# Kernel optimization log

Measured on AMD Instinct MI355X. Metric: run time of the kernel, lower is better.

Reference implementation:

```python
import jax, jax.numpy as jnp
import numpy as np

NUM_EXPERTS = 8
TOP_K = 2
D_MODEL = 1024
EXPERT_CAP = 512  # dim_feedforward // num_experts = 4096 // 8
B, S = 4, 2048


def setup_inputs() -> dict:
    key = jax.random.key(0)
    ks = jax.random.split(key, 4)
    scale = 1.0 / np.sqrt(D_MODEL)
    x = jax.random.normal(ks[0], (B, S, D_MODEL), dtype=jnp.float32)
    gate_w = jax.random.normal(ks[1], (D_MODEL, NUM_EXPERTS), dtype=jnp.float32) * scale
    w1 = jax.random.normal(ks[2], (NUM_EXPERTS, D_MODEL, EXPERT_CAP), dtype=jnp.float32) * scale
    b1 = jnp.zeros((NUM_EXPERTS, EXPERT_CAP), dtype=jnp.float32)
    w2 = jax.random.normal(ks[3], (NUM_EXPERTS, EXPERT_CAP, D_MODEL), dtype=jnp.float32) * (1.0 / np.sqrt(EXPERT_CAP))
    b2 = jnp.zeros((NUM_EXPERTS, D_MODEL), dtype=jnp.float32)
    return {"x": x, "gate_w": gate_w, "w1": w1, "b1": b1, "w2": w2, "b2": b2}


def reference(x, gate_w, w1, b1, w2, b2):
    Bx, Sx, D = x.shape
    xt = x.reshape(-1, D)  # [N, D], N = B*S
    gates = jax.nn.softmax(xt @ gate_w, axis=-1)           # [N, E]
    topk_g, topk_i = jax.lax.top_k(gates, TOP_K)           # [N, K]
    # Faithful to source: every selected expert is scaled by the SUM of all top-k gates
    tok_w = topk_g.sum(axis=-1)                            # [N]
    sel = (topk_i[:, :, None] == jnp.arange(NUM_EXPERTS)[None, None, :]).any(axis=1)  # [N, E] bool
    # Dense per-expert MLP (E small), then mask-combine (scatter-add equivalent)
    h = jax.nn.gelu(jnp.einsum('nd,edh->enh', xt, w1) + b1[:, None, :], approximate=False)  # [E, N, H]
    y = jnp.einsum('enh,ehd->end', h, w2) + b2[:, None, :]  # [E, N, D]
    out = jnp.einsum('end,ne,n->nd', y, sel.astype(x.dtype), tok_w)  # [N, D]
    return out.reshape(Bx, Sx, D)
```

## Files before the change

kernel.cpp:

```cpp
#include <hip/hip_runtime.h>
#include <math.h>

#define N_TOK 8192
#define DM 1024
#define NE 8
#define HE 512
#define NPAIR 16384
#define MAXMB 264

#define BM 64
#define BN 128
#define BK 64
#define OSTR 136

#define GSTR 1028

typedef __bf16 bf16x8 __attribute__((ext_vector_type(8)));
typedef float f32x4 __attribute__((ext_vector_type(4)));

#define GLOBAL_AS __attribute__((address_space(1)))
#define LDS_AS    __attribute__((address_space(3)))

__device__ __forceinline__ void gl_lds16(const void* g, void* lds) {
    __builtin_amdgcn_global_load_lds((const GLOBAL_AS unsigned int*)g,
                                     (LDS_AS unsigned int*)lds, 16, 0, 0);
}

__device__ __forceinline__ unsigned short f2bf(float f) {
    unsigned int u = __float_as_uint(f);
    u += 0x7fffu + ((u >> 16) & 1u);
    return (unsigned short)(u >> 16);
}

__device__ __forceinline__ float gelu_exact(float v) {
    return 0.5f * v * (1.0f + erff(v * 0.70710678118654752440f));
}

__device__ __forceinline__ double shfl_xor_dbl(double v, int m) {
    long long l = __double_as_longlong(v);
    int lo = (int)(l & 0xffffffffll);
    int hi = (int)(l >> 32);
    lo = __shfl_xor(lo, m, 64);
    hi = __shfl_xor(hi, m, 64);
    return __longlong_as_double(((long long)hi << 32) | (unsigned long long)(unsigned int)lo);
}

__global__ __launch_bounds__(256) void prep_kernel(
        const float* __restrict__ x, const float* __restrict__ gw,
        const float* __restrict__ w1, const float* __restrict__ w2,
        unsigned short* __restrict__ xb,
        unsigned short* __restrict__ w1t, unsigned short* __restrict__ w2t,
        float* __restrict__ w_tok, int* __restrict__ e_sel) {
    __shared__ float smf[NE * GSTR];
    int bid = blockIdx.x;
    int tid = threadIdx.x;

    if (bid >= 2048) {
        int t = bid - 2048;
        int z = t >> 7;
        int idx = t & 127;
        int bx = idx & 7, by = idx >> 3;
        const float* src; unsigned short* dst; int R, C, c0, r0;
        if (z < 8) {
            src = w1 + (size_t)z * DM * HE; dst = w1t + (size_t)z * DM * HE;
            R = DM; C = HE; c0 = bx * 64; r0 = by * 64;
        } else {
            int e = z - 8;
            src = w2 + (size_t)e * HE * DM; dst = w2t + (size_t)e * HE * DM;
            R = HE; C = DM; c0 = by * 64; r0 = bx * 64;
        }
        float (*tile)[65] = (float(*)[65])smf;
        int tc = tid & 63, tg = tid >> 6;
        #pragma unroll
        for (int i = 0; i < 16; i++) {
            int r = tg * 16 + i;
            tile[r][tc] = src[(size_t)(r0 + r) * C + (c0 + tc)];
        }
        __syncthreads();
        #pragma unroll
        for (int i = 0; i < 16; i++) {
            int r = tg * 16 + i;
            dst[(size_t)(c0 + r) * R + (r0 + tc)] = f2bf(tile[tc][r]);
        }
        return;
    }

    float* gls = smf;
    for (int v = tid; v < 2048; v += 256) {
        float4 g4 = ((const float4*)gw)[v];
        int idx = v * 4;
        int d = idx >> 3;
        int e0 = idx & 7;
        gls[(e0    ) * GSTR + d] = g4.x;
        gls[(e0 + 1) * GSTR + d] = g4.y;
        gls[(e0 + 2) * GSTR + d] = g4.z;
        gls[(e0 + 3) * GSTR + d] = g4.w;
    }
    __syncthreads();

    int n = bid * 4 + (tid >> 6);
    int lane = tid & 63;
    const float4* xr = (const float4*)(x + (size_t)n * DM);
    ushort4* xw = (ushort4*)(xb + (size_t)n * DM);

    double s[NE];
    #pragma unroll
    for (int e = 0; e < NE; e++) s[e] = 0.0;

    #pragma unroll
    for (int i = 0; i < 4; i++) {
        float4 x4 = xr[i * 64 + lane];
        ushort4 o;
        o.x = f2bf(x4.x); o.y = f2bf(x4.y); o.z = f2bf(x4.z); o.w = f2bf(x4.w);
        xw[i * 64 + lane] = o;
        int d = (i * 64 + lane) * 4;
        #pragma unroll
        for (int e = 0; e < NE; e++) {
            float4 g4 = *(const float4*)(&gls[e * GSTR + d]);
            s[e] += (double)x4.x * (double)g4.x + (double)x4.y * (double)g4.y
                  + (double)x4.z * (double)g4.z + (double)x4.w * (double)g4.w;
        }
    }
    #pragma unroll
    for (int e = 0; e < NE; e++) {
        for (int off = 32; off > 0; off >>= 1)
            s[e] += shfl_xor_dbl(s[e], off);
    }
    if (lane == 0) {
        double m = s[0];
        for (int e = 1; e < NE; e++) if (s[e] > m) m = s[e];
        double sum = 0.0;
        for (int e = 0; e < NE; e++) sum += exp(s[e] - m);
        int i1 = 0; double v1 = s[0];
        for (int e = 1; e < NE; e++) if (s[e] > v1) { v1 = s[e]; i1 = e; }
        int i2 = -1; double v2 = -1e300;
        for (int e = 0; e < NE; e++) if (e != i1 && s[e] > v2) { v2 = s[e]; i2 = e; }
        w_tok[n] = (float)((exp(v1 - m) + exp(v2 - m)) / sum);
        e_sel[2 * n]     = i1;
        e_sel[2 * n + 1] = i2;
    }
}

__global__ __launch_bounds__(1024) void route_kernel(
        const int* __restrict__ e_sel, int* __restrict__ cnt, int* __restrict__ offs,
        int* __restrict__ pair_tok, int* __restrict__ slotmap,
        int* __restrict__ mb_e, int* __restrict__ mb_base, int* __restrict__ n_mb) {
    __shared__ int wbin[16][NE];
    __shared__ int wstart[16][NE];
    __shared__ int etot[NE], eoffs[NE], bofs[NE];
    int tid = threadIdx.x;
    int w = tid >> 6, l = tid & 63;
    if (l < NE) wbin[w][l] = 0;
    __syncthreads();

    int sel[16];
    #pragma unroll
    for (int k = 0; k < 16; k++) {
        sel[k] = e_sel[tid * 16 + k];
        atomicAdd(&wbin[w][sel[k]], 1);
    }
    __syncthreads();

    if (tid < NE) {
        int t = 0;
        for (int ww = 0; ww < 16; ww++) t += wbin[ww][tid];
        etot[tid] = t;
    }
    __syncthreads();
    if (tid == 0) {
        int a = 0, b = 0;
        for (int e = 0; e < NE; e++) {
            eoffs[e] = a; a += etot[e];
            bofs[e] = b;  b += (etot[e] + BM - 1) / BM;
        }
        n_mb[0] = b;
    }
    __syncthreads();
    if (tid < NE) {
        cnt[tid] = etot[tid];
        offs[tid] = eoffs[tid];
        int r = eoffs[tid];
        for (int ww = 0; ww < 16; ww++) { wstart[ww][tid] = r; r += wbin[ww][tid]; }
        int nb = (etot[tid] + BM - 1) / BM;
        int b0 = bofs[tid];
        for (int b = 0; b < nb; b++) {
            mb_e[b0 + b] = tid;
            mb_base[b0 + b] = eoffs[tid] + b * BM;
        }
    }
    __syncthreads();
    if (l < NE) wbin[w][l] = wstart[w][l];
    __syncthreads();

    #pragma unroll
    for (int k = 0; k < 16; k++) {
        int i = tid * 16 + k;
        int slot = atomicAdd(&wbin[w][sel[k]], 1);
        pair_tok[slot] = i >> 1;
        slotmap[i] = slot;
    }
}

__global__ __launch_bounds__(256, 4) void gemm1_kernel(
        const unsigned short* __restrict__ xb,
        const unsigned short* __restrict__ w1t,
        const float* __restrict__ b1,
        const int* __restrict__ pair_tok,
        const int* __restrict__ cnt, const int* __restrict__ offs,
        const int* __restrict__ mb_e, const int* __restrict__ mb_base,
        const int* __restrict__ n_mb,
        unsigned short* __restrict__ hbuf) {
    int mb = blockIdx.y;
    if (mb >= n_mb[0]) return;
    int e = mb_e[mb];
    int sbase = mb_base[mb];
    int vlim = offs[e] + cnt[e];
    int n0 = blockIdx.x * BN;

    __shared__ __align__(16) unsigned short smem[BM * BK + BN * BK];
    char* As = (char*)smem;
    char* Bs = (char*)smem + 8192;

    int tid = threadIdx.x;
    int lane = tid & 63;
    int w = tid >> 6;
    int wu = __builtin_amdgcn_readfirstlane(w);
    int l3 = lane >> 3, l7 = lane & 7;
    int g = l7 ^ l3;

    const char* aptr[2];
    const char* bptr[4];
    #pragma unroll
    for (int j = 0; j < 2; j++) {
        int row = w * 16 + j * 8 + l3;
        int slot = sbase + row;
        int t = pair_tok[slot < vlim ? slot : vlim - 1];
        aptr[j] = (const char*)xb + (size_t)t * (DM * 2) + g * 16;
    }
    #pragma unroll
    for (int j = 0; j < 4; j++) {
        int row = w * 32 + j * 8 + l3;
        bptr[j] = (const char*)w1t + ((size_t)e * HE + n0 + row) * (DM * 2) + g * 16;
    }

    int wm = (w & 1) * 32;
    int wn = (w >> 1) * 64;
    int fr = lane & 15;
    int fq = lane >> 4;

    f32x4 acc[2][4];
    #pragma unroll
    for (int i = 0; i < 2; i++)
        #pragma unroll
        for (int j = 0; j < 4; j++)
            acc[i][j] = (f32x4){0.f, 0.f, 0.f, 0.f};

    for (int k0 = 0; k0 < DM; k0 += BK) {
        int kb = k0 * 2;
        #pragma unroll
        for (int j = 0; j < 2; j++)
            gl_lds16(aptr[j] + kb, As + wu * 2048 + j * 1024);
        #pragma unroll
        for (int j = 0; j < 4; j++)
            gl_lds16(bptr[j] + kb, Bs + wu * 4096 + j * 1024);
        __syncthreads();
        #pragma unroll
        for (int kk2 = 0; kk2 < 2; kk2++) {
            int sw = ((kk2 * 4 + fq) ^ (fr & 7)) << 4;
            bf16x8 af[2], bfv[4];
            #pragma unroll
            for (int i = 0; i < 2; i++)
                af[i] = *(const bf16x8*)(As + (wm + i * 16 + fr) * 128 + sw);
            #pragma unroll
            for (int j = 0; j < 4; j++)
                bfv[j] = *(const bf16x8*)(Bs + (wn + j * 16 + fr) * 128 + sw);
            #pragma unroll
            for (int i = 0; i < 2; i++)
                #pragma unroll
                for (int j = 0; j < 4; j++)
                    acc[i][j] = __builtin_amdgcn_mfma_f32_16x16x32_bf16(af[i], bfv[j], acc[i][j], 0, 0, 0);
        }
        __syncthreads();
    }

    unsigned short* ot = smem;
    #pragma unroll
    for (int j = 0; j < 4; j++) {
        int nl = wn + j * 16 + fr;
        float bias = b1[e * HE + n0 + nl];
        #pragma unroll
        for (int i = 0; i < 2; i++) {
            #pragma unroll
            for (int r = 0; r < 4; r++) {
                int mm = wm + i * 16 + fq * 4 + r;
                ot[mm * OSTR + nl] = f2bf(gelu_exact(acc[i][j][r] + bias));
            }
        }
    }
    __syncthreads();
    int row = tid >> 2;
    int c0 = (tid & 3) * 32;
    if (sbase + row < vlim) {
        const uint4* sp = (const uint4*)(ot + row * OSTR + c0);
        uint4* dp = (uint4*)(hbuf + (size_t)(sbase + row) * HE + n0 + c0);
        dp[0] = sp[0]; dp[1] = sp[1]; dp[2] = sp[2]; dp[3] = sp[3];
    }
}

__global__ __launch_bounds__(256, 4) void gemm2_kernel(
        const unsigned short* __restrict__ hbuf,
        const unsigned short* __restrict__ w2t,
        const float* __restrict__ b2,
        const int* __restrict__ pair_tok,
        const float* __restrict__ w_tok,
        const int* __restrict__ cnt, const int* __restrict__ offs,
        const int* __restrict__ mb_e, const int* __restrict__ mb_base,
        const int* __restrict__ n_mb,
        unsigned short* __restrict__ ybuf) {
    int mb = blockIdx.y;
    if (mb >= n_mb[0]) return;
    int e = mb_e[mb];
    int sbase = mb_base[mb];
    int vlim = offs[e] + cnt[e];
    int n0 = blockIdx.x * BN;

    __shared__ __align__(16) unsigned short smem[BM * BK + BN * BK];
    char* As = (char*)smem;
    char* Bs = (char*)smem + 8192;
    __shared__ float wts[BM];

    int tid = threadIdx.x;
    if (tid < BM) {
        int slot = sbase + tid;
        wts[tid] = w_tok[pair_tok[slot < vlim ? slot : vlim - 1]];
    }
    __syncthreads();

    int lane = tid & 63;
    int w = tid >> 6;
    int wu = __builtin_amdgcn_readfirstlane(w);
    int l3 = lane >> 3, l7 = lane & 7;
    int g = l7 ^ l3;

    const char* aptr[2];
    const char* bptr[4];
    #pragma unroll
    for (int j = 0; j < 2; j++) {
        int row = w * 16 + j * 8 + l3;
        int slot = sbase + row;
        int cs = (slot < vlim) ? slot : vlim - 1;
        aptr[j] = (const char*)hbuf + (size_t)cs * (HE * 2) + g * 16;
    }
    #pragma unroll
    for (int j = 0; j < 4; j++) {
        int row = w * 32 + j * 8 + l3;
        bptr[j] = (const char*)w2t + ((size_t)e * DM + n0 + row) * (HE * 2) + g * 16;
    }

    int wm = (w & 1) * 32;
    int wn = (w >> 1) * 64;
    int fr = lane & 15;
    int fq = lane >> 4;

    f32x4 acc[2][4];
    #pragma unroll
    for (int i = 0; i < 2; i++)
        #pragma unroll
        for (int j = 0; j < 4; j++)
            acc[i][j] = (f32x4){0.f, 0.f, 0.f, 0.f};

    for (int k0 = 0; k0 < HE; k0 += BK) {
        int kb = k0 * 2;
        #pragma unroll
        for (int j = 0; j < 2; j++)
            gl_lds16(aptr[j] + kb, As + wu * 2048 + j * 1024);
        #pragma unroll
        for (int j = 0; j < 4; j++)
            gl_lds16(bptr[j] + kb, Bs + wu * 4096 + j * 1024);
        __syncthreads();
        #pragma unroll
        for (int kk2 = 0; kk2 < 2; kk2++) {
            int sw = ((kk2 * 4 + fq) ^ (fr & 7)) << 4;
            bf16x8 af[2], bfv[4];
            #pragma unroll
            for (int i = 0; i < 2; i++)
                af[i] = *(const bf16x8*)(As + (wm + i * 16 + fr) * 128 + sw);
            #pragma unroll
            for (int j = 0; j < 4; j++)
                bfv[j] = *(const bf16x8*)(Bs + (wn + j * 16 + fr) * 128 + sw);
            #pragma unroll
            for (int i = 0; i < 2; i++)
                #pragma unroll
                for (int j = 0; j < 4; j++)
                    acc[i][j] = __builtin_amdgcn_mfma_f32_16x16x32_bf16(af[i], bfv[j], acc[i][j], 0, 0, 0);
        }
        __syncthreads();
    }

    unsigned short* ot = smem;
    #pragma unroll
    for (int j = 0; j < 4; j++) {
        int nl = wn + j * 16 + fr;
        float bias = b2[e * DM + n0 + nl];
        #pragma unroll
        for (int i = 0; i < 2; i++) {
            #pragma unroll
            for (int r = 0; r < 4; r++) {
                int mm = wm + i * 16 + fq * 4 + r;
                ot[mm * OSTR + nl] = f2bf(wts[mm] * (acc[i][j][r] + bias));
            }
        }
    }
    __syncthreads();
    int row = tid >> 2;
    int c0 = (tid & 3) * 32;
    if (sbase + row < vlim) {
        const uint4* sp = (const uint4*)(ot + row * OSTR + c0);
        uint4* dp = (uint4*)(ybuf + (size_t)(sbase + row) * DM + n0 + c0);
        dp[0] = sp[0]; dp[1] = sp[1]; dp[2] = sp[2]; dp[3] = sp[3];
    }
}

__device__ __forceinline__ float2 bfpair(unsigned int u) {
    float2 f;
    f.x = __uint_as_float(u << 16);
    f.y = __uint_as_float(u & 0xffff0000u);
    return f;
}

__global__ void combine_kernel(const unsigned short* __restrict__ yb,
                               const int* __restrict__ slotmap,
                               float* __restrict__ out) {
    int i = blockIdx.x * 256 + threadIdx.x;
    int n = i >> 7;
    int c = (i & 127) * 8;
    int s1 = slotmap[2 * n];
    int s2 = slotmap[2 * n + 1];
    uint4 a = *(const uint4*)(&yb[(size_t)s1 * DM + c]);
    uint4 b = *(const uint4*)(&yb[(size_t)s2 * DM + c]);
    float2 ax = bfpair(a.x), ay = bfpair(a.y), az = bfpair(a.z), aw = bfpair(a.w);
    float2 bx = bfpair(b.x), by = bfpair(b.y), bz = bfpair(b.z), bw = bfpair(b.w);
    float4 o0, o1;
    o0.x = ax.x + bx.x; o0.y = ax.y + bx.y; o0.z = ay.x + by.x; o0.w = ay.y + by.y;
    o1.x = az.x + bz.x; o1.y = az.y + bz.y; o1.z = aw.x + bw.x; o1.w = aw.y + bw.y;
    float4* dp = (float4*)(out + (size_t)n * DM + c);
    dp[0] = o0; dp[1] = o1;
}

extern "C" void kernel_launch(void* const* d_in, const int* in_sizes, int n_in,
                              void* d_out, int out_size, void* d_ws, size_t ws_size,
                              hipStream_t stream) {
    const float* x  = (const float*)d_in[0];
    const float* gw = (const float*)d_in[1];
    const float* w1 = (const float*)d_in[2];
    const float* b1 = (const float*)d_in[3];
    const float* w2 = (const float*)d_in[4];
    const float* b2 = (const float*)d_in[5];
    float* out = (float*)d_out;

    char* ws = (char*)d_ws;
    unsigned short* ybuf = (unsigned short*)(ws);
    unsigned short* xb   = (unsigned short*)(ws);
    unsigned short* w1t  = (unsigned short*)(ws + 16777216);
    unsigned short* w2t  = (unsigned short*)(ws + 33554432);
    unsigned short* hbuf = (unsigned short*)(ws + 41943040);
    float* w_tok         = (float*)(ws + 58720256);
    int*   e_sel         = (int*)(ws + 58753024);
    int*   slotmap       = (int*)(ws + 58818560);
    int*   cnt           = (int*)(ws + 58884096);
    int*   offs          = (int*)(ws + 58884128);
    int*   pair_tok      = (int*)(ws + 58884224);
    int*   mb_e          = (int*)(ws + 58949760);
    int*   mb_base       = (int*)(ws + 58950848);
    int*   n_mb          = (int*)(ws + 58951936);

    prep_kernel<<<4096, 256, 0, stream>>>(x, gw, w1, w2, xb, w1t, w2t, w_tok, e_sel);
    route_kernel<<<1, 1024, 0, stream>>>(e_sel, cnt, offs, pair_tok, slotmap,
                                         mb_e, mb_base, n_mb);
    gemm1_kernel<<<dim3(HE / BN, MAXMB), 256, 0, stream>>>(
        xb, w1t, b1, pair_tok, cnt, offs, mb_e, mb_base, n_mb, hbuf);
    gemm2_kernel<<<dim3(DM / BN, MAXMB), 256, 0, stream>>>(
        hbuf, w2t, b2, pair_tok, w_tok, cnt, offs, mb_e, mb_base, n_mb, ybuf);
    combine_kernel<<<(N_TOK * DM / 8) / 256, 256, 0, stream>>>(ybuf, slotmap, out);
}
```

Baseline: 222.0 us.

## Enlarge GEMM1 K-tile, widen GEMM2 N-tile, move token weight to combine

GEMM1 now stages a 128-wide K slice per iteration, halving the number of barrier-separated loop steps, and lowers its launch bound from 4 to 3 blocks per CU to fit the larger LDS footprint. GEMM2 widens its output tile to 256 columns, so each A tile is reused across more MFMAs and half as many blocks are launched, at the cost of more accumulator registers. The per-token gate weight multiply moves from the GEMM2 epilogue into the combine kernel, which removes an LDS weight table and a barrier from GEMM2. The risks are lower occupancy and register pressure in both GEMMs.

```diff
diff --git a/kernel.cpp b/kernel.cpp
--- a/kernel.cpp
+++ b/kernel.cpp
@@ -9,9 +9,8 @@
 #define MAXMB 264
 
 #define BM 64
-#define BN 128
-#define BK 64
 #define OSTR 136
+#define OSTR2 264
 
 #define GSTR 1028
 
@@ -201,7 +200,7 @@
     }
 }
 
-__global__ __launch_bounds__(256, 4) void gemm1_kernel(
+__global__ __launch_bounds__(256, 3) void gemm1_kernel(
         const unsigned short* __restrict__ xb,
         const unsigned short* __restrict__ w1t,
         const float* __restrict__ b1,
@@ -215,32 +214,35 @@
     int e = mb_e[mb];
     int sbase = mb_base[mb];
     int vlim = offs[e] + cnt[e];
-    int n0 = blockIdx.x * BN;
-
-    __shared__ __align__(16) unsigned short smem[BM * BK + BN * BK];
+    int n0 = blockIdx.x * 128;
+
+    __shared__ __align__(16) unsigned short smem[(64 + 128) * 128];
     char* As = (char*)smem;
-    char* Bs = (char*)smem + 8192;
+    char* Bs = (char*)smem + 16384;
 
     int tid = threadIdx.x;
     int lane = tid & 63;
     int w = tid >> 6;
     int wu = __builtin_amdgcn_readfirstlane(w);
-    int l3 = lane >> 3, l7 = lane & 7;
-    int g = l7 ^ l3;
-
-    const char* aptr[2];
-    const char* bptr[4];
-    #pragma unroll
-    for (int j = 0; j < 2; j++) {
-        int row = w * 16 + j * 8 + l3;
-        int slot = sbase + row;
+    int r16 = lane >> 4;
+    int s7  = lane & 7;
+    int hb  = ((lane >> 3) & 1) * 128;
+
+    const char* aptr[4];
+    #pragma unroll
+    for (int j = 0; j < 4; j++) {
+        int rl = w * 16 + j * 4 + r16;
+        int slot = sbase + rl;
         int t = pair_tok[slot < vlim ? slot : vlim - 1];
-        aptr[j] = (const char*)xb + (size_t)t * (DM * 2) + g * 16;
-    }
-    #pragma unroll
-    for (int j = 0; j < 4; j++) {
-        int row = w * 32 + j * 8 + l3;
-        bptr[j] = (const char*)w1t + ((size_t)e * HE + n0 + row) * (DM * 2) + g * 16;
+        int sub = s7 ^ (rl & 7);
+        aptr[j] = (const char*)xb + (size_t)t * (DM * 2) + hb + sub * 16;
+    }
+    const char* bptr[8];
+    #pragma unroll
+    for (int j = 0; j < 8; j++) {
+        int rl = w * 32 + j * 4 + r16;
+        int sub = s7 ^ (rl & 7);
+        bptr[j] = (const char*)w1t + ((size_t)e * HE + n0 + rl) * (DM * 2) + hb + sub * 16;
     }
 
     int wm = (w & 1) * 32;
@@ -255,30 +257,29 @@
         for (int j = 0; j < 4; j++)
             acc[i][j] = (f32x4){0.f, 0.f, 0.f, 0.f};
 
-    for (int k0 = 0; k0 < DM; k0 += BK) {
+    for (int k0 = 0; k0 < DM; k0 += 128) {
         int kb = k0 * 2;
         #pragma unroll
-        for (int j = 0; j < 2; j++)
-            gl_lds16(aptr[j] + kb, As + wu * 2048 + j * 1024);
-        #pragma unroll
         for (int j = 0; j < 4; j++)
-            gl_lds16(bptr[j] + kb, Bs + wu * 4096 + j * 1024);
+            gl_lds16(aptr[j] + kb, As + wu * 4096 + j * 1024);
+        #pragma unroll
+        for (int j = 0; j < 8; j++)
+            gl_lds16(bptr[j] + kb, Bs + wu * 8192 + j * 1024);
         __syncthreads();
         #pragma unroll
-        for (int kk2 = 0; kk2 < 2; kk2++) {
-            int sw = ((kk2 * 4 + fq) ^ (fr & 7)) << 4;
-            bf16x8 af[2], bfv[4];
+        for (int kk = 0; kk < 4; kk++) {
+            int off = (kk >> 1) * 128 + ((((kk & 1) * 4 + fq) ^ (fr & 7)) << 4);
+            bf16x8 af[2];
             #pragma unroll
             for (int i = 0; i < 2; i++)
-                af[i] = *(const bf16x8*)(As + (wm + i * 16 + fr) * 128 + sw);
-            #pragma unroll
-            for (int j = 0; j < 4; j++)
-                bfv[j] = *(const bf16x8*)(Bs + (wn + j * 16 + fr) * 128 + sw);
-            #pragma unroll
-            for (int i = 0; i < 2; i++)
+                af[i] = *(const bf16x8*)(As + (wm + i * 16 + fr) * 256 + off);
+            #pragma unroll
+            for (int j = 0; j < 4; j++) {
+                bf16x8 bfv = *(const bf16x8*)(Bs + (wn + j * 16 + fr) * 256 + off);
                 #pragma unroll
-                for (int j = 0; j < 4; j++)
-                    acc[i][j] = __builtin_amdgcn_mfma_f32_16x16x32_bf16(af[i], bfv[j], acc[i][j], 0, 0, 0);
+                for (int i = 0; i < 2; i++)
+                    acc[i][j] = __builtin_amdgcn_mfma_f32_16x16x32_bf16(af[i], bfv, acc[i][j], 0, 0, 0);
+            }
         }
         __syncthreads();
     }
@@ -312,7 +313,6 @@
         const unsigned short* __restrict__ w2t,
         const float* __restrict__ b2,
         const int* __restrict__ pair_tok,
-        const float* __restrict__ w_tok,
         const int* __restrict__ cnt, const int* __restrict__ offs,
         const int* __restrict__ mb_e, const int* __restrict__ mb_base,
         const int* __restrict__ n_mb,
@@ -322,20 +322,13 @@
     int e = mb_e[mb];
     int sbase = mb_base[mb];
     int vlim = offs[e] + cnt[e];
-    int n0 = blockIdx.x * BN;
-
-    __shared__ __align__(16) unsigned short smem[BM * BK + BN * BK];
+    int n0 = blockIdx.x * 256;
+
+    __shared__ __align__(16) unsigned short smem[(64 + 256) * 64];
     char* As = (char*)smem;
     char* Bs = (char*)smem + 8192;
-    __shared__ float wts[BM];
 
     int tid = threadIdx.x;
-    if (tid < BM) {
-        int slot = sbase + tid;
-        wts[tid] = w_tok[pair_tok[slot < vlim ? slot : vlim - 1]];
-    }
-    __syncthreads();
-
     int lane = tid & 63;
     int w = tid >> 6;
     int wu = __builtin_amdgcn_readfirstlane(w);
@@ -343,63 +336,62 @@
     int g = l7 ^ l3;
 
     const char* aptr[2];
-    const char* bptr[4];
     #pragma unroll
     for (int j = 0; j < 2; j++) {
-        int row = w * 16 + j * 8 + l3;
-        int slot = sbase + row;
+        int rl = w * 16 + j * 8 + l3;
+        int slot = sbase + rl;
         int cs = (slot < vlim) ? slot : vlim - 1;
         aptr[j] = (const char*)hbuf + (size_t)cs * (HE * 2) + g * 16;
     }
-    #pragma unroll
-    for (int j = 0; j < 4; j++) {
-        int row = w * 32 + j * 8 + l3;
-        bptr[j] = (const char*)w2t + ((size_t)e * DM + n0 + row) * (HE * 2) + g * 16;
+    const char* bptr[8];
+    #pragma unroll
+    for (int j = 0; j < 8; j++) {
+        int rl = w * 64 + j * 8 + l3;
+        bptr[j] = (const char*)w2t + ((size_t)e * DM + n0 + rl) * (HE * 2) + g * 16;
     }
 
     int wm = (w & 1) * 32;
-    int wn = (w >> 1) * 64;
+    int wn = (w >> 1) * 128;
     int fr = lane & 15;
     int fq = lane >> 4;
 
-    f32x4 acc[2][4];
+    f32x4 acc[2][8];
     #pragma unroll
     for (int i = 0; i < 2; i++)
         #pragma unroll
-        for (int j = 0; j < 4; j++)
+        for (int j = 0; j < 8; j++)
             acc[i][j] = (f32x4){0.f, 0.f, 0.f, 0.f};
 
-    for (int k0 = 0; k0 < HE; k0 += BK) {
+    for (int k0 = 0; k0 < HE; k0 += 64) {
         int kb = k0 * 2;
         #pragma unroll
         for (int j = 0; j < 2; j++)
             gl_lds16(aptr[j] + kb, As + wu * 2048 + j * 1024);
         #pragma unroll
-        for (int j = 0; j < 4; j++)
-            gl_lds16(bptr[j] + kb, Bs + wu * 4096 + j * 1024);
+        for (int j = 0; j < 8; j++)
+            gl_lds16(bptr[j] + kb, Bs + wu * 8192 + j * 1024);
         __syncthreads();
         #pragma unroll
         for (int kk2 = 0; kk2 < 2; kk2++) {
             int sw = ((kk2 * 4 + fq) ^ (fr & 7)) << 4;
-            bf16x8 af[2], bfv[4];
+            bf16x8 af[2];
             #pragma unroll
             for (int i = 0; i < 2; i++)
                 af[i] = *(const bf16x8*)(As + (wm + i * 16 + fr) * 128 + sw);
             #pragma unroll
-            for (int j = 0; j < 4; j++)
-                bfv[j] = *(const bf16x8*)(Bs + (wn + j * 16 + fr) * 128 + sw);
-            #pragma unroll
-            for (int i = 0; i < 2; i++)
+            for (int j = 0; j < 8; j++) {
+                bf16x8 bfv = *(const bf16x8*)(Bs + (wn + j * 16 + fr) * 128 + sw);
                 #pragma unroll
-                for (int j = 0; j < 4; j++)
-                    acc[i][j] = __builtin_amdgcn_mfma_f32_16x16x32_bf16(af[i], bfv[j], acc[i][j], 0, 0, 0);
+                for (int i = 0; i < 2; i++)
+                    acc[i][j] = __builtin_amdgcn_mfma_f32_16x16x32_bf16(af[i], bfv, acc[i][j], 0, 0, 0);
+            }
         }
         __syncthreads();
     }
 
     unsigned short* ot = smem;
     #pragma unroll
-    for (int j = 0; j < 4; j++) {
+    for (int j = 0; j < 8; j++) {
         int nl = wn + j * 16 + fr;
         float bias = b2[e * DM + n0 + nl];
         #pragma unroll
@@ -407,17 +399,21 @@
             #pragma unroll
             for (int r = 0; r < 4; r++) {
                 int mm = wm + i * 16 + fq * 4 + r;
-                ot[mm * OSTR + nl] = f2bf(wts[mm] * (acc[i][j][r] + bias));
+                ot[mm * OSTR2 + nl] = f2bf(acc[i][j][r] + bias);
             }
         }
     }
     __syncthreads();
     int row = tid >> 2;
-    int c0 = (tid & 3) * 32;
-    if (sbase + row < vlim) {
-        const uint4* sp = (const uint4*)(ot + row * OSTR + c0);
-        uint4* dp = (uint4*)(ybuf + (size_t)(sbase + row) * DM + n0 + c0);
-        dp[0] = sp[0]; dp[1] = sp[1]; dp[2] = sp[2]; dp[3] = sp[3];
+    bool live = (sbase + row < vlim);
+    #pragma unroll
+    for (int p = 0; p < 2; p++) {
+        int c0 = p * 128 + (tid & 3) * 32;
+        if (live) {
+            const uint4* sp = (const uint4*)(ot + row * OSTR2 + c0);
+            uint4* dp = (uint4*)(ybuf + (size_t)(sbase + row) * DM + n0 + c0);
+            dp[0] = sp[0]; dp[1] = sp[1]; dp[2] = sp[2]; dp[3] = sp[3];
+        }
     }
 }
 
@@ -430,19 +426,23 @@
 
 __global__ void combine_kernel(const unsigned short* __restrict__ yb,
                                const int* __restrict__ slotmap,
+                               const float* __restrict__ w_tok,
                                float* __restrict__ out) {
     int i = blockIdx.x * 256 + threadIdx.x;
     int n = i >> 7;
     int c = (i & 127) * 8;
     int s1 = slotmap[2 * n];
     int s2 = slotmap[2 * n + 1];
+    float wt = w_tok[n];
     uint4 a = *(const uint4*)(&yb[(size_t)s1 * DM + c]);
     uint4 b = *(const uint4*)(&yb[(size_t)s2 * DM + c]);
     float2 ax = bfpair(a.x), ay = bfpair(a.y), az = bfpair(a.z), aw = bfpair(a.w);
     float2 bx = bfpair(b.x), by = bfpair(b.y), bz = bfpair(b.z), bw = bfpair(b.w);
     float4 o0, o1;
-    o0.x = ax.x + bx.x; o0.y = ax.y + bx.y; o0.z = ay.x + by.x; o0.w = ay.y + by.y;
-    o1.x = az.x + bz.x; o1.y = az.y + bz.y; o1.z = aw.x + bw.x; o1.w = aw.y + bw.y;
+    o0.x = wt * (ax.x + bx.x); o0.y = wt * (ax.y + bx.y);
+    o0.z = wt * (ay.x + by.x); o0.w = wt * (ay.y + by.y);
+    o1.x = wt * (az.x + bz.x); o1.y = wt * (az.y + bz.y);
+    o1.z = wt * (aw.x + bw.x); o1.w = wt * (aw.y + bw.y);
     float4* dp = (float4*)(out + (size_t)n * DM + c);
     dp[0] = o0; dp[1] = o1;
 }
@@ -477,9 +477,9 @@
     prep_kernel<<<4096, 256, 0, stream>>>(x, gw, w1, w2, xb, w1t, w2t, w_tok, e_sel);
     route_kernel<<<1, 1024, 0, stream>>>(e_sel, cnt, offs, pair_tok, slotmap,
                                          mb_e, mb_base, n_mb);
-    gemm1_kernel<<<dim3(HE / BN, MAXMB), 256, 0, stream>>>(
+    gemm1_kernel<<<dim3(HE / 128, MAXMB), 256, 0, stream>>>(
         xb, w1t, b1, pair_tok, cnt, offs, mb_e, mb_base, n_mb, hbuf);
-    gemm2_kernel<<<dim3(DM / BN, MAXMB), 256, 0, stream>>>(
-        hbuf, w2t, b2, pair_tok, w_tok, cnt, offs, mb_e, mb_base, n_mb, ybuf);
-    combine_kernel<<<(N_TOK * DM / 8) / 256, 256, 0, stream>>>(ybuf, slotmap, out);
-}
+    gemm2_kernel<<<dim3(DM / 256, MAXMB), 256, 0, stream>>>(
+        hbuf, w2t, b2, pair_tok, cnt, offs, mb_e, mb_base, n_mb, ybuf);
+    combine_kernel<<<(N_TOK * DM / 8) / 256, 256, 0, stream>>>(ybuf, slotmap, w_tok, out);
+}
```

Measured after the change: 232.8 us. 4.9% more time.
